# Performance work log

Measured on AMD Instinct MI355X. Metric: run time of the kernel, lower is better.

The kernel has to match this reference:

```python
import jax, jax.numpy as jnp
import numpy as np

IN_DIM, H, D = 45, 128, 256

def setup_inputs() -> dict:
    key = jax.random.key(0)
    ks = jax.random.split(key, 9)
    s_in = 1.0 / np.sqrt(IN_DIM)
    s_h = 1.0 / np.sqrt(H)
    return {
        "pose": jax.random.normal(ks[0], (64, 4096, 9, 5), dtype=jnp.float32),
        "ln1_g": jnp.ones((IN_DIM,), jnp.float32),
        "ln1_b": jnp.zeros((IN_DIM,), jnp.float32),
        "w1": jax.random.uniform(ks[1], (IN_DIM, H), jnp.float32, -s_in, s_in),
        "b1": jax.random.uniform(ks[2], (H,), jnp.float32, -s_in, s_in),
        "w2": jax.random.uniform(ks[3], (H, D), jnp.float32, -s_h, s_h),
        "b2": jax.random.uniform(ks[4], (D,), jnp.float32, -s_h, s_h),
        "ln2_g": jnp.ones((D,), jnp.float32),
        "ln2_b": jnp.zeros((D,), jnp.float32),
    }

def _layernorm(x, g, b, eps=1e-5):
    mu = jnp.mean(x, axis=-1, keepdims=True)
    var = jnp.mean(jnp.square(x - mu), axis=-1, keepdims=True)
    return (x - mu) * jax.lax.rsqrt(var + eps) * g + b

def reference(pose, ln1_g, ln1_b, w1, b1, w2, b2, ln2_g, ln2_b):
    B, T, J, C = pose.shape
    x = pose.reshape(B, T, J * C)                      # [B,T,45]
    x = _layernorm(x, ln1_g, ln1_b)
    x = jnp.einsum('btf,fh->bth', x, w1) + b1          # [B,T,128]
    x = jax.nn.gelu(x, approximate=False)              # torch GELU default = exact erf
    # dropout is identity in eval mode
    x = jnp.einsum('bth,hd->btd', x, w2) + b2          # [B,T,256]
    return _layernorm(x, ln2_g, ln2_b)
```

## Files before the change

kernel.cpp:

```cpp
#include <hip/hip_runtime.h>
#include <cstdint>

#define IN_DIM 45
#define HDIM 128
#define DDIM 256
#define ROWS 64
#define NBLK 4096

typedef unsigned short u16;
typedef __attribute__((ext_vector_type(8))) short v8s;
typedef __attribute__((ext_vector_type(4))) float f32x4;

__device__ __forceinline__ u16 f2bf(float x){
  uint32_t u = __float_as_uint(x);
  u += 0x7FFFu + ((u >> 16) & 1u);
  return (u16)(u >> 16);
}

__device__ __forceinline__ void g2l16(const void* g, void* l){
  __builtin_amdgcn_global_load_lds(
      (const __attribute__((address_space(1))) unsigned int*)g,
      (__attribute__((address_space(3))) unsigned int*)l, 16, 0, 0);
}

__global__ void prep_kernel(const float* __restrict__ w1, const float* __restrict__ w2,
                            u16* __restrict__ w1s, u16* __restrict__ w2s){
  int idx = blockIdx.x*256 + threadIdx.x;
  if (idx < 128*64){
    int n = idx >> 6, k = idx & 63;
    int gp = (k >> 3) ^ (n & 7);
    float v = (k < IN_DIM) ? w1[k*HDIM + n] : 0.f;
    w1s[(n << 6) | (gp << 3) | (k & 7)] = f2bf(v);
  } else if (idx < 128*64 + 256*128){
    int t = idx - 128*64;
    int n = t >> 7, k = t & 127;
    int gp = ((k >> 3) ^ (n & 15));
    w2s[(n << 7) | (gp << 3) | (k & 7)] = f2bf(w2[k*DDIM + n]);
  }
}

__global__ __launch_bounds__(256, 2)
void posemlp_kernel(const float* __restrict__ pose,
                    const float* __restrict__ ln1g, const float* __restrict__ ln1b,
                    const float* __restrict__ b1v,  const float* __restrict__ b2v,
                    const float* __restrict__ ln2g, const float* __restrict__ ln2b,
                    const u16* __restrict__ w1s, const u16* __restrict__ w2s,
                    float* __restrict__ out)
{
  __shared__ __align__(16) unsigned char smem[43008];
  u16*  sw = (u16*)smem;
  u16*  sx = (u16*)(smem + 16384);
  u16*  sh = (u16*)(smem + 25600);
  float* posel = (float*)(smem + 25600);

  const int tid = threadIdx.x;
  const int blk = blockIdx.x;

  {
    const char* psrc = (const char*)pose + (size_t)blk * (ROWS*IN_DIM*4);
    #pragma unroll
    for (int j = 0; j < 3; ++j){
      int i = j*256 + tid;
      if (i < 720) g2l16(psrc + (size_t)i*16, smem + 25600 + i*16);
    }
    const char* wsrc = (const char*)w1s;
    #pragma unroll
    for (int j = 0; j < 4; ++j){
      int i = j*256 + tid;
      g2l16(wsrc + (size_t)i*16, smem + i*16);
    }
  }
  __syncthreads();

  {
    int row = tid >> 2, p = tid & 3;
    const float* pr = posel + row*IN_DIM;
    float sum = 0.f, sq = 0.f;
    for (int k = p; k < IN_DIM; k += 4){ float v = pr[k]; sum += v; sq += v*v; }
    sum += __shfl_xor(sum, 1); sum += __shfl_xor(sum, 2);
    sq  += __shfl_xor(sq, 1);  sq  += __shfl_xor(sq, 2);
    float mu = sum * (1.f/IN_DIM);
    float rs = rsqrtf(sq * (1.f/IN_DIM) - mu*mu + 1e-5f);
    u16* xr = sx + row*72;
    for (int k = p; k < IN_DIM; k += 4){
      float v = (pr[k] - mu) * rs * ln1g[k] + ln1b[k];
      xr[k] = f2bf(v);
    }
    for (int k = IN_DIM + p; k < 64; k += 4) xr[k] = 0;
  }
  __syncthreads();

  const int lane = tid & 63, wv = tid >> 6;
  const int col = lane & 15, quad = lane >> 4;

  f32x4 acc1[8];
  #pragma unroll
  for (int i = 0; i < 8; ++i) acc1[i] = (f32x4){0.f,0.f,0.f,0.f};
  {
    const u16* xa = sx + (16*wv + col)*72;
    #pragma unroll
    for (int ks = 0; ks < 2; ++ks){
      v8s a = *(const v8s*)(xa + ks*32 + quad*8);
      #pragma unroll
      for (int nt = 0; nt < 8; ++nt){
        int n = nt*16 + col;
        int gp = (ks*4 + quad) ^ (n & 7);
        v8s b = *(const v8s*)(sw + n*64 + gp*8);
        acc1[nt] = __builtin_amdgcn_mfma_f32_16x16x32_bf16(a, b, acc1[nt], 0, 0, 0);
      }
    }
  }
  #pragma unroll
  for (int nt = 0; nt < 8; ++nt){
    int n = nt*16 + col;
    float bias = b1v[n];
    #pragma unroll
    for (int r = 0; r < 4; ++r){
      float v = acc1[nt][r] + bias;
      v = 0.5f * v * (1.f + erff(v * 0.70710678118654752f));
      sh[(16*wv + quad*4 + r)*136 + n] = f2bf(v);
    }
  }
  __syncthreads();

  v8s a2[4];
  {
    const u16* ha = sh + (16*wv + col)*136;
    #pragma unroll
    for (int ks = 0; ks < 4; ++ks) a2[ks] = *(const v8s*)(ha + ks*32 + quad*8);
  }

  f32x4 acc2[16];
  #pragma unroll
  for (int i = 0; i < 16; ++i) acc2[i] = (f32x4){0.f,0.f,0.f,0.f};
  const char* w2b = (const char*)w2s;
  #pragma unroll
  for (int hq = 0; hq < 4; ++hq){
    #pragma unroll
    for (int j = 0; j < 4; ++j){
      int i = j*256 + tid;
      g2l16(w2b + (size_t)hq*16384 + (size_t)i*16, smem + i*16);
    }
    __syncthreads();
    #pragma unroll
    for (int ntl = 0; ntl < 4; ++ntl){
      int nq = ntl*16 + col;
      #pragma unroll
      for (int ks = 0; ks < 4; ++ks){
        int gp = (ks*4 + quad) ^ (nq & 15);
        v8s b = *(const v8s*)(sw + nq*128 + gp*8);
        acc2[hq*4 + ntl] = __builtin_amdgcn_mfma_f32_16x16x32_bf16(a2[ks], b, acc2[hq*4 + ntl], 0, 0, 0);
      }
    }
    __syncthreads();
  }

  float sum[4] = {0,0,0,0}, sq[4] = {0,0,0,0};
  #pragma unroll
  for (int i = 0; i < 16; ++i){
    float bb = b2v[i*16 + col];
    #pragma unroll
    for (int r = 0; r < 4; ++r){
      float v = acc2[i][r] + bb;
      acc2[i][r] = v;
      sum[r] += v; sq[r] += v*v;
    }
  }
  #pragma unroll
  for (int m = 1; m <= 8; m <<= 1){
    #pragma unroll
    for (int r = 0; r < 4; ++r){
      sum[r] += __shfl_xor(sum[r], m);
      sq[r]  += __shfl_xor(sq[r], m);
    }
  }
  float mu[4], rs[4];
  #pragma unroll
  for (int r = 0; r < 4; ++r){
    mu[r] = sum[r] * (1.f/DDIM);
    rs[r] = rsqrtf(sq[r] * (1.f/DDIM) - mu[r]*mu[r] + 1e-5f);
  }
  const int rbase = blk*ROWS + 16*wv + quad*4;
  #pragma unroll
  for (int r = 0; r < 4; ++r){
    #pragma unroll
    for (int i = 0; i < 16; ++i){
      int n = i*16 + col;
      out[(size_t)(rbase + r)*DDIM + n] =
          (acc2[i][r] - mu[r]) * rs[r] * ln2g[n] + ln2b[n];
    }
  }
}

extern "C" void kernel_launch(void* const* d_in, const int* in_sizes, int n_in,
                              void* d_out, int out_size, void* d_ws, size_t ws_size,
                              hipStream_t stream){
  const float* pose = (const float*)d_in[0];
  const float* ln1g = (const float*)d_in[1];
  const float* ln1b = (const float*)d_in[2];
  const float* w1   = (const float*)d_in[3];
  const float* b1   = (const float*)d_in[4];
  const float* w2   = (const float*)d_in[5];
  const float* b2   = (const float*)d_in[6];
  const float* ln2g = (const float*)d_in[7];
  const float* ln2b = (const float*)d_in[8];
  u16* w1s = (u16*)d_ws;
  u16* w2s = (u16*)((char*)d_ws + 16384);
  prep_kernel<<<160, 256, 0, stream>>>(w1, w2, w1s, w2s);
  posemlp_kernel<<<NBLK, 256, 0, stream>>>(pose, ln1g, ln1b, b1, b2, ln2g, ln2b,
                                           w1s, w2s, (float*)d_out);
}
```

Before: 393.3 us.

## Transpose MFMA operands, double-buffer W2 in LDS, read W1 from global

The MFMA operands are swapped so weights form the A side and activations the B side. Each lane then owns whole output rows, which allows float4 bias loads, row-local layernorm reductions with fewer shuffles, and vectorized float4 output stores. W1 is read straight from global memory instead of LDS, which removes one barrier. W2 is staged through a double buffer whose next quarter is prefetched while the current one is consumed. LDS use grows to about 70KB per block, which can lower occupancy below the two blocks per CU requested by launch bounds.

After: 406.1 us. +3.3%, slower.

```diff
diff --git a/kernel.cpp b/kernel.cpp
--- a/kernel.cpp
+++ b/kernel.cpp
@@ -2,8 +2,6 @@
 #include <cstdint>
 
 #define IN_DIM 45
-#define HDIM 128
-#define DDIM 256
 #define ROWS 64
 #define NBLK 4096
 
@@ -28,14 +26,13 @@
   int idx = blockIdx.x*256 + threadIdx.x;
   if (idx < 128*64){
     int n = idx >> 6, k = idx & 63;
-    int gp = (k >> 3) ^ (n & 7);
-    float v = (k < IN_DIM) ? w1[k*HDIM + n] : 0.f;
-    w1s[(n << 6) | (gp << 3) | (k & 7)] = f2bf(v);
+    float v = (k < IN_DIM) ? w1[k*128 + n] : 0.f;
+    w1s[idx] = f2bf(v);
   } else if (idx < 128*64 + 256*128){
-    int t = idx - 128*64;
+    int t = idx - 8192;
     int n = t >> 7, k = t & 127;
-    int gp = ((k >> 3) ^ (n & 15));
-    w2s[(n << 7) | (gp << 3) | (k & 7)] = f2bf(w2[k*DDIM + n]);
+    int gp = (k >> 3) ^ (n & 15);
+    w2s[(n << 7) | (gp << 3) | (k & 7)] = f2bf(w2[k*256 + n]);
   }
 }
 
@@ -47,11 +44,11 @@
                     const u16* __restrict__ w1s, const u16* __restrict__ w2s,
                     float* __restrict__ out)
 {
-  __shared__ __align__(16) unsigned char smem[43008];
-  u16*  sw = (u16*)smem;
-  u16*  sx = (u16*)(smem + 16384);
-  u16*  sh = (u16*)(smem + 25600);
-  float* posel = (float*)(smem + 25600);
+  __shared__ __align__(16) unsigned char smem[70912];
+  u16*  swbuf = (u16*)smem;
+  u16*  sx = (u16*)(smem + 32768);
+  u16*  sh = (u16*)(smem + 41984);
+  float* posel = (float*)(smem + 59392);
 
   const int tid = threadIdx.x;
   const int blk = blockIdx.x;
@@ -61,13 +58,13 @@
     #pragma unroll
     for (int j = 0; j < 3; ++j){
       int i = j*256 + tid;
-      if (i < 720) g2l16(psrc + (size_t)i*16, smem + 25600 + i*16);
+      if (i < 720) g2l16(psrc + i*16, smem + 59392 + i*16);
     }
-    const char* wsrc = (const char*)w1s;
+    const char* wsrc = (const char*)w2s;
     #pragma unroll
-    for (int j = 0; j < 4; ++j){
+    for (int j = 0; j < 8; ++j){
       int i = j*256 + tid;
-      g2l16(wsrc + (size_t)i*16, smem + i*16);
+      g2l16(wsrc + i*16, smem + i*16);
     }
   }
   __syncthreads();
@@ -82,13 +79,10 @@
     float mu = sum * (1.f/IN_DIM);
     float rs = rsqrtf(sq * (1.f/IN_DIM) - mu*mu + 1e-5f);
     u16* xr = sx + row*72;
-    for (int k = p; k < IN_DIM; k += 4){
-      float v = (pr[k] - mu) * rs * ln1g[k] + ln1b[k];
-      xr[k] = f2bf(v);
-    }
+    for (int k = p; k < IN_DIM; k += 4)
+      xr[k] = f2bf((pr[k] - mu) * rs * ln1g[k] + ln1b[k]);
     for (int k = IN_DIM + p; k < 64; k += 4) xr[k] = 0;
   }
-  __syncthreads();
 
   const int lane = tid & 63, wv = tid >> 6;
   const int col = lane & 15, quad = lane >> 4;
@@ -97,98 +91,87 @@
   #pragma unroll
   for (int i = 0; i < 8; ++i) acc1[i] = (f32x4){0.f,0.f,0.f,0.f};
   {
-    const u16* xa = sx + (16*wv + col)*72;
+    const u16* xa = sx + (16*wv + col)*72 + quad*8;
+    v8s bx0 = *(const v8s*)(xa);
+    v8s bx1 = *(const v8s*)(xa + 32);
     #pragma unroll
-    for (int ks = 0; ks < 2; ++ks){
-      v8s a = *(const v8s*)(xa + ks*32 + quad*8);
-      #pragma unroll
-      for (int nt = 0; nt < 8; ++nt){
-        int n = nt*16 + col;
-        int gp = (ks*4 + quad) ^ (n & 7);
-        v8s b = *(const v8s*)(sw + n*64 + gp*8);
-        acc1[nt] = __builtin_amdgcn_mfma_f32_16x16x32_bf16(a, b, acc1[nt], 0, 0, 0);
-      }
+    for (int nt = 0; nt < 8; ++nt){
+      const u16* wr = w1s + (nt*16 + col)*64 + quad*8;
+      v8s a0 = *(const v8s*)(wr);
+      v8s a1 = *(const v8s*)(wr + 32);
+      acc1[nt] = __builtin_amdgcn_mfma_f32_16x16x32_bf16(a0, bx0, acc1[nt], 0, 0, 0);
+      acc1[nt] = __builtin_amdgcn_mfma_f32_16x16x32_bf16(a1, bx1, acc1[nt], 0, 0, 0);
     }
   }
   #pragma unroll
   for (int nt = 0; nt < 8; ++nt){
-    int n = nt*16 + col;
-    float bias = b1v[n];
+    float4 bb = ((const float4*)b1v)[nt*4 + quad];
+    float v0 = acc1[nt][0] + bb.x, v1 = acc1[nt][1] + bb.y;
+    float v2 = acc1[nt][2] + bb.z, v3 = acc1[nt][3] + bb.w;
+    v0 = 0.5f*v0*(1.f + erff(v0*0.70710678118654752f));
+    v1 = 0.5f*v1*(1.f + erff(v1*0.70710678118654752f));
+    v2 = 0.5f*v2*(1.f + erff(v2*0.70710678118654752f));
+    v3 = 0.5f*v3*(1.f + erff(v3*0.70710678118654752f));
+    ushort4 pk; pk.x = f2bf(v0); pk.y = f2bf(v1); pk.z = f2bf(v2); pk.w = f2bf(v3);
+    *(ushort4*)(sh + (16*wv + col)*136 + nt*16 + quad*4) = pk;
+  }
+  v8s bh[4];
+  {
+    const u16* ha = sh + (16*wv + col)*136 + quad*8;
     #pragma unroll
-    for (int r = 0; r < 4; ++r){
-      float v = acc1[nt][r] + bias;
-      v = 0.5f * v * (1.f + erff(v * 0.70710678118654752f));
-      sh[(16*wv + quad*4 + r)*136 + n] = f2bf(v);
-    }
-  }
-  __syncthreads();
-
-  v8s a2[4];
-  {
-    const u16* ha = sh + (16*wv + col)*136;
-    #pragma unroll
-    for (int ks = 0; ks < 4; ++ks) a2[ks] = *(const v8s*)(ha + ks*32 + quad*8);
+    for (int ks = 0; ks < 4; ++ks) bh[ks] = *(const v8s*)(ha + ks*32);
   }
 
   f32x4 acc2[16];
   #pragma unroll
   for (int i = 0; i < 16; ++i) acc2[i] = (f32x4){0.f,0.f,0.f,0.f};
-  const char* w2b = (const char*)w2s;
   #pragma unroll
   for (int hq = 0; hq < 4; ++hq){
-    #pragma unroll
-    for (int j = 0; j < 4; ++j){
-      int i = j*256 + tid;
-      g2l16(w2b + (size_t)hq*16384 + (size_t)i*16, smem + i*16);
-    }
-    __syncthreads();
+    const u16* sw = swbuf + (hq & 1)*8192;
     #pragma unroll
     for (int ntl = 0; ntl < 4; ++ntl){
-      int nq = ntl*16 + col;
+      const u16* wr = sw + (ntl*16 + col)*128;
       #pragma unroll
       for (int ks = 0; ks < 4; ++ks){
-        int gp = (ks*4 + quad) ^ (nq & 15);
-        v8s b = *(const v8s*)(sw + nq*128 + gp*8);
-        acc2[hq*4 + ntl] = __builtin_amdgcn_mfma_f32_16x16x32_bf16(a2[ks], b, acc2[hq*4 + ntl], 0, 0, 0);
+        v8s a = *(const v8s*)(wr + (((ks*4 + quad) ^ col) << 3));
+        acc2[hq*4 + ntl] = __builtin_amdgcn_mfma_f32_16x16x32_bf16(a, bh[ks], acc2[hq*4 + ntl], 0, 0, 0);
       }
     }
-    __syncthreads();
+    if (hq < 3) __syncthreads();
+    if (hq < 2){
+      const char* src = (const char*)w2s + (hq + 2)*16384;
+      #pragma unroll
+      for (int j = 0; j < 4; ++j){
+        int i = j*256 + tid;
+        g2l16(src + i*16, smem + (hq & 1)*16384 + i*16);
+      }
+    }
   }
 
-  float sum[4] = {0,0,0,0}, sq[4] = {0,0,0,0};
+  float sum = 0.f, sq = 0.f;
   #pragma unroll
   for (int i = 0; i < 16; ++i){
-    float bb = b2v[i*16 + col];
-    #pragma unroll
-    for (int r = 0; r < 4; ++r){
-      float v = acc2[i][r] + bb;
-      acc2[i][r] = v;
-      sum[r] += v; sq[r] += v*v;
-    }
+    float4 bb = ((const float4*)b2v)[i*4 + quad];
+    acc2[i][0] += bb.x; acc2[i][1] += bb.y; acc2[i][2] += bb.z; acc2[i][3] += bb.w;
+    sum += acc2[i][0] + acc2[i][1] + acc2[i][2] + acc2[i][3];
+    sq  += acc2[i][0]*acc2[i][0] + acc2[i][1]*acc2[i][1]
+         + acc2[i][2]*acc2[i][2] + acc2[i][3]*acc2[i][3];
   }
+  sum += __shfl_xor(sum, 16); sum += __shfl_xor(sum, 32);
+  sq  += __shfl_xor(sq, 16);  sq  += __shfl_xor(sq, 32);
+  float mu = sum * (1.f/256.f);
+  float rs = rsqrtf(sq * (1.f/256.f) - mu*mu + 1e-5f);
+  float* orow = out + (size_t)(blk*ROWS + 16*wv + col)*256;
   #pragma unroll
-  for (int m = 1; m <= 8; m <<= 1){
-    #pragma unroll
-    for (int r = 0; r < 4; ++r){
-      sum[r] += __shfl_xor(sum[r], m);
-      sq[r]  += __shfl_xor(sq[r], m);
-    }
-  }
-  float mu[4], rs[4];
-  #pragma unroll
-  for (int r = 0; r < 4; ++r){
-    mu[r] = sum[r] * (1.f/DDIM);
-    rs[r] = rsqrtf(sq[r] * (1.f/DDIM) - mu[r]*mu[r] + 1e-5f);
-  }
-  const int rbase = blk*ROWS + 16*wv + quad*4;
-  #pragma unroll
-  for (int r = 0; r < 4; ++r){
-    #pragma unroll
-    for (int i = 0; i < 16; ++i){
-      int n = i*16 + col;
-      out[(size_t)(rbase + r)*DDIM + n] =
-          (acc2[i][r] - mu[r]) * rs[r] * ln2g[n] + ln2b[n];
-    }
+  for (int i = 0; i < 16; ++i){
+    float4 g = ((const float4*)ln2g)[i*4 + quad];
+    float4 b = ((const float4*)ln2b)[i*4 + quad];
+    float4 o;
+    o.x = (acc2[i][0] - mu)*rs*g.x + b.x;
+    o.y = (acc2[i][1] - mu)*rs*g.y + b.y;
+    o.z = (acc2[i][2] - mu)*rs*g.z + b.z;
+    o.w = (acc2[i][3] - mu)*rs*g.w + b.w;
+    ((float4*)orow)[i*4 + quad] = o;
   }
 }
 
```
